# Optimization experiments

Hardware: AMD Instinct MI355X
Metric: run time of the kernel (lower is better)

Reference implementation:

```python
import jax, jax.numpy as jnp
import numpy as np

B, N, K, CIN, COUT, H = 4, 2048, 32, 16, 32, 32
EPS = 1e-5


def setup_inputs() -> dict:
    key = jax.random.key(0)
    ks = jax.random.split(key, 6)
    s = 0.1
    return dict(
        xyz=jax.random.uniform(ks[0], (B, N, 3), dtype=jnp.float32),
        points=jax.random.normal(ks[1], (B, N, CIN), dtype=jnp.float32),
        W1=jax.random.normal(ks[2], (3, H), dtype=jnp.float32) * s,
        b1=jnp.zeros((H,), jnp.float32),
        g1=jnp.ones((H,), jnp.float32),
        be1=jnp.zeros((H,), jnp.float32),
        W2=jax.random.normal(ks[3], (H, H), dtype=jnp.float32) * s,
        b2=jnp.zeros((H,), jnp.float32),
        g2=jnp.ones((H,), jnp.float32),
        be2=jnp.zeros((H,), jnp.float32),
        W3=jax.random.normal(ks[4], (H, CIN * COUT), dtype=jnp.float32) * s,
        b3=jnp.zeros((CIN * COUT,), jnp.float32),
        gbn=jnp.ones((COUT,), jnp.float32),
        bbn=jnp.zeros((COUT,), jnp.float32),
    )


def _bn(h, g, b):
    # BatchNorm1d training-mode math: biased batch stats over axis 0
    return g * (h - h.mean(0)) / jnp.sqrt(h.var(0) + EPS) + b


def reference(xyz, points, W1, b1, g1, be1, W2, b2, g2, be2, W3, b3, gbn, bbn):
    # KNN: squared distances (B,N,N)
    sq = jnp.sum(xyz * xyz, -1)
    dist = -2.0 * jnp.einsum('bmc,bnc->bmn', xyz, xyz) + sq[:, :, None] + sq[:, None, :]
    _, idx = jax.lax.top_k(-dist, K)  # (B,N,K) nearest neighbors

    gather = jax.vmap(lambda p, i: p[i])  # (N,C),(N,K)->(N,K,C), vmapped over B
    grouped_xyz = gather(xyz, idx)                      # (B,N,K,3)
    rel = grouped_xyz - xyz[:, :, None, :]              # (B,N,K,3)
    grouped_pts = gather(points, idx)                   # (B,N,K,CIN)

    # weight net on relative coords
    h = rel.reshape(-1, 3)
    h = _bn(jax.nn.relu(h @ W1 + b1), g1, be1)
    h = _bn(jax.nn.relu(h @ W2 + b2), g2, be2)
    w = (h @ W3 + b3).reshape(B, N, K, CIN, COUT)       # (B,N,K,CIN,COUT)

    # weighted sum over C_in, then max over neighbors
    out = jnp.einsum('bnkc,bnkco->bnko', grouped_pts, w)  # (B,N,K,COUT)
    out = out.max(axis=2)                                 # (B,N,COUT)

    # final BatchNorm1d over (B,N) per channel
    m = out.mean((0, 1))
    v = out.var((0, 1))
    return gbn * (out - m) / jnp.sqrt(v + EPS) + bbn
```

## Files before the change

kernel.cpp:

```cpp
#include <hip/hip_runtime.h>

#define B_ 4
#define N_ 2048
#define K_ 32
#define CIN_ 16
#define COUT_ 32
#define H_ 32
#define R_ (B_*N_*K_)
#define EPS_ 1e-5f
#define INVR_ (1.0f/(float)R_)
#define INVBN_ (1.0f/(float)(B_*N_))
#define LISTCAP 192

typedef __attribute__((ext_vector_type(8)))  _Float16 f16x8;
typedef __attribute__((ext_vector_type(2)))  __fp16   hw16x2;
typedef __attribute__((ext_vector_type(2)))  _Float16 f16x2;
typedef __attribute__((ext_vector_type(16))) float    f32x16;

__device__ __forceinline__ float dot3f(float ax,float ay,float az,float bx,float by,float bz){
    return fmaf(az,bz, fmaf(ay,by, ax*bx));
}
__device__ __forceinline__ unsigned int flip_f32(float d){
    unsigned int u = __float_as_uint(d);
    return u ^ ((unsigned int)(((int)u) >> 31) | 0x80000000u);
}
__device__ __forceinline__ unsigned int pk2(float a, float b){
    union { hw16x2 v; unsigned int u; } c;
    c.v = __builtin_amdgcn_cvt_pkrtz(a, b);
    return c.u;
}
__device__ __forceinline__ unsigned int pkmul(unsigned int a, unsigned int b){
    union { unsigned int u; f16x2 v; } x, y, r;
    x.u = a; y.u = b; r.v = x.v * y.v; return r.u;
}
__device__ __forceinline__ float sh8(const float* __restrict__ p, int k){
    float s = 0.f;
    #pragma unroll
    for (int i = 0; i < 8; ++i) s += p[i*32 + k];
    return s;
}

__device__ __forceinline__ void hsel4(const unsigned int* hq , int lane,
                                      unsigned int Kthr, int* Bsel, unsigned int* below){
    unsigned int g[4];
    #pragma unroll
    for (int t = 0; t < 4; ++t){
        uint4 h = ((const uint4*)hq)[4*lane + t];
        g[t] = h.x + h.y + h.z + h.w;
    }
    unsigned int gs = g[0]+g[1]+g[2]+g[3], cum = gs;
    #pragma unroll
    for (int off = 1; off < 64; off <<= 1){
        unsigned int v = __shfl_up(cum, off);
        if (lane >= off) cum += v;
    }
    unsigned long long bal = __ballot(cum >= Kthr);
    int L = __ffsll(bal) - 1;
    unsigned int run = __shfl(cum, L) - __shfl(gs, L);
    unsigned int h0 = __shfl(g[0], L), h1 = __shfl(g[1], L), h2 = __shfl(g[2], L);
    if      (run + h0 >= Kthr)           { *Bsel = 4*L;     *below = run; }
    else if (run + h0 + h1 >= Kthr)      { *Bsel = 4*L + 1; *below = run + h0; }
    else if (run + h0 + h1 + h2 >= Kthr) { *Bsel = 4*L + 2; *below = run + h0 + h1; }
    else                                 { *Bsel = 4*L + 3; *below = run + h0 + h1 + h2; }
}

__global__ __launch_bounds__(256) void k_prep0(const float* __restrict__ xyz, float4* __restrict__ xs4g,
                                               float* __restrict__ st){
    int i = blockIdx.x*256 + threadIdx.x;
    float x = xyz[3*i], y = xyz[3*i+1], z = xyz[3*i+2];
    xs4g[i] = make_float4(x, y, z, dot3f(x,y,z,x,y,z));
    if (blockIdx.x == 0){
        for (int j = threadIdx.x; j < 640; j += 256) st[j] = 0.f;
    }
}

__global__ __launch_bounds__(256) void k_knn(const float4* __restrict__ xs4g,
                                             const float* __restrict__ W1, const float* __restrict__ b1,
                                             int* __restrict__ idx_out,
                                             float* __restrict__ s1sh, float* __restrict__ q1sh){
    __shared__ unsigned int hist[2][256][4];
    __shared__ unsigned long long lst[2][LISTCAP];
    __shared__ int kidx[2][K_];
    __shared__ unsigned int cnt[2];
    __shared__ float sacc[H_], qacc[H_];

    const int tid  = threadIdx.x;
    const int w    = tid >> 6;
    const int lane = tid & 63;
    const int qi   = w >> 1;
    const int lq   = tid & 127;
    const int b    = blockIdx.x / (N_/2);
    const int q    = (blockIdx.x % (N_/2)) * 2 + qi;
    const int bN   = b * N_;

    for (int i = tid; i < 2048; i += 256) ((unsigned int*)hist)[i] = 0u;
    if (tid < 2) cnt[tid] = 0u;
    if (tid < H_){ sacc[tid] = 0.f; qacc[tid] = 0.f; }
    __syncthreads();

    const float4 qp = xs4g[bN + q];
    const float qx = qp.x, qy = qp.y, qz = qp.z, sqq = qp.w;

    unsigned int fv[16];
    #pragma unroll
    for (int j = 0; j < 16; ++j){
        int c = j*128 + lq;
        float4 pt = xs4g[bN + c];
        float d = fmaf(-2.0f, dot3f(qx,qy,qz, pt.x,pt.y,pt.z), sqq) + pt.w;
        unsigned int f = flip_f32(d);
        fv[j] = f;
        atomicAdd(&hist[qi][f >> 24][lane & 3], 1u);
    }
    __syncthreads();

    int B0; unsigned int lt0;
    hsel4(&hist[qi][0][0], lane, (unsigned)K_, &B0, &lt0);
    unsigned int Kp = (unsigned)K_ - lt0;
    __syncthreads();

    for (int i = tid; i < 2048; i += 256) ((unsigned int*)hist)[i] = 0u;
    __syncthreads();

    #pragma unroll
    for (int j = 0; j < 16; ++j){
        if ((int)(fv[j] >> 24) == B0)
            atomicAdd(&hist[qi][(fv[j] >> 16) & 0xFF][lane & 3], 1u);
    }
    __syncthreads();

    int B1s; unsigned int lt1;
    hsel4(&hist[qi][0][0], lane, Kp, &B1s, &lt1);

    const unsigned long long mlt = (lane == 63) ? ~0ull >> 1 : (1ull << lane) - 1ull;
    #pragma unroll
    for (int j = 0; j < 16; ++j){
        unsigned int f = fv[j];
        int top = (int)(f >> 24);
        bool surv = (top < B0) || (top == B0 && (int)((f >> 16) & 0xFF) <= B1s);
        unsigned long long sb = __ballot(surv);
        if (sb){
            unsigned int t = (unsigned int)__popcll(sb);
            unsigned int base;
            if (lane == 0) base = atomicAdd(&cnt[qi], t);
            base = __shfl(base, 0, 64);
            unsigned int pos = base + (unsigned int)__popcll(sb & mlt);
            if (surv && pos < (unsigned)LISTCAP)
                lst[qi][pos] = ((unsigned long long)f << 32) | (unsigned int)(j*128 + lq);
        }
    }
    __syncthreads();

    int m = (int)cnt[qi]; if (m > LISTCAP) m = LISTCAP;

    int* outp = idx_out + ((size_t)bN + q) * K_;
    for (int i = lq; i < m; i += 128){
        unsigned long long my = lst[qi][i];
        int rank = 0;
        for (int jj = 0; jj < m; ++jj)
            rank += (lst[qi][jj] < my) ? 1 : 0;
        if (rank < K_){
            int id = (int)(unsigned int)(my & 0xFFFFFFFFull);
            outp[rank] = id;
            kidx[qi][rank] = id;
        }
    }
    __syncthreads();

    {
        const int ch = lq & 31, rg = lq >> 5;
        float w1a = W1[ch], w1b = W1[H_+ch], w1c = W1[2*H_+ch], b1c = b1[ch];
        float s = 0.f, qq = 0.f;
        #pragma unroll
        for (int r = 0; r < 8; ++r){
            int id = kidx[qi][rg*8 + r];
            float4 pn = xs4g[bN + id];
            float rx = pn.x - qx, ry = pn.y - qy, rz = pn.z - qz;
            float h = fmaxf(fmaf(rx, w1a, fmaf(ry, w1b, fmaf(rz, w1c, b1c))), 0.0f);
            s += h; qq = fmaf(h, h, qq);
        }
        s  += __shfl_xor(s, 32, 64);
        qq += __shfl_xor(qq, 32, 64);
        if (lane < 32){ atomicAdd(&sacc[lane], s); atomicAdd(&qacc[lane], qq); }
    }
    __syncthreads();
    if (tid < H_){
        int sh = (blockIdx.x & 7) * 32 + tid;
        atomicAdd(&s1sh[sh], sacc[tid]);
        atomicAdd(&q1sh[sh], qacc[tid]);
    }
}

__device__ __forceinline__ void compute_h1(const float* __restrict__ xyz, const int* __restrict__ idx, int r,
                                           const float* __restrict__ W1, const float* __restrict__ b1, float* h1){
    int b = r >> 16;
    int n = (r >> 5) & (N_-1);
    int id = idx[r];
    const float* pc = xyz + ((size_t)b*N_ + n)*3;
    const float* pn = xyz + ((size_t)b*N_ + id)*3;
    float rx = pn[0]-pc[0], ry = pn[1]-pc[1], rz = pn[2]-pc[2];
    #pragma unroll
    for (int j = 0; j < H_; ++j){
        float a = fmaf(rx, W1[j], fmaf(ry, W1[H_+j], fmaf(rz, W1[2*H_+j], b1[j])));
        h1[j] = fmaxf(a, 0.0f);
    }
}

__global__ __launch_bounds__(256) void k_prep2(const float* __restrict__ points,
                                               const float* __restrict__ s1s, const float* __restrict__ q1s,
                                               const float* __restrict__ g1, const float* __restrict__ be1,
                                               const float* __restrict__ W2, const float* __restrict__ b2,
                                               unsigned int* __restrict__ pf16, unsigned int* __restrict__ W2f,
                                               float* __restrict__ b2p){
    int flat = blockIdx.x*256 + threadIdx.x;
    if (flat < 65536){
        pf16[flat] = pk2(points[2*flat], points[2*flat+1]);
    } else if (flat < 66048){
        int d = flat - 65536;
        int jj = d & 3, lane = (d >> 2) & 63, step = d >> 8;
        int col = lane & 31;
        int k0 = step*16 + (lane >> 5)*8 + 2*jj;
        float m0 = sh8(s1s,k0)*INVR_,   v0 = sh8(q1s,k0)*INVR_   - m0*m0;
        float m1 = sh8(s1s,k0+1)*INVR_, v1 = sh8(q1s,k0+1)*INVR_ - m1*m1;
        float a0  = g1[k0]   / sqrtf(v0 + EPS_);
        float a1v = g1[k0+1] / sqrtf(v1 + EPS_);
        W2f[d] = pk2(a0*W2[k0*H_ + col], a1v*W2[(k0+1)*H_ + col]);
    } else if (flat < 66080){
        int col = flat - 66048;
        float acc = b2[col];
        #pragma unroll 4
        for (int h = 0; h < H_; ++h){
            float mm = sh8(s1s,h)*INVR_, vv = sh8(q1s,h)*INVR_ - mm*mm;
            float aa = g1[h] / sqrtf(vv + EPS_);
            float bb = fmaf(-aa, mm, be1[h]);
            acc = fmaf(bb, W2[h*H_ + col], acc);
        }
        b2p[col] = acc;
    }
}

__global__ __launch_bounds__(256,3) void k_h2(const float* __restrict__ xyz, const int* __restrict__ idx,
                                              const float* __restrict__ W1, const float* __restrict__ b1,
                                              const uint4* __restrict__ W2f, const float* __restrict__ b2p,
                                              unsigned short* __restrict__ h2g,
                                              float* gsum, float* gsq){
    __shared__ float redS[H_], redQ[H_];
    const int tid = threadIdx.x, lane = tid & 63, w = tid >> 6;
    const int half = lane >> 5, m = lane & 31;
    if (tid < H_){ redS[tid] = 0.f; redQ[tid] = 0.f; }
    __syncthreads();

    int r = blockIdx.x*256 + tid;
    float h1[H_];
    compute_h1(xyz, idx, r, W1, b1, h1);
    unsigned int h1p[16];
    #pragma unroll
    for (int i = 0; i < 16; ++i) h1p[i] = pk2(h1[2*i], h1[2*i+1]);

    union { uint4 u4; f16x8 v; } Bf0, Bf1;
    Bf0.u4 = W2f[lane];
    Bf1.u4 = W2f[64 + lane];
    float b2c = b2p[m];

    const int rB = blockIdx.x*256 + w*64;
    float s = 0.f, q = 0.f;
    #pragma unroll
    for (int t = 0; t < 2; ++t){
        const int src = t*32 + m;
        union { unsigned int u[4]; f16x8 v; } a0, a1f;
        #pragma unroll
        for (int jj = 0; jj < 4; ++jj){
            unsigned int lo = __shfl(h1p[jj],     src, 64);
            unsigned int hi = __shfl(h1p[4 + jj], src, 64);
            a0.u[jj] = half ? hi : lo;
        }
        #pragma unroll
        for (int jj = 0; jj < 4; ++jj){
            unsigned int lo = __shfl(h1p[8 + jj],  src, 64);
            unsigned int hi = __shfl(h1p[12 + jj], src, 64);
            a1f.u[jj] = half ? hi : lo;
        }
        f32x16 acc;
        #pragma unroll
        for (int i = 0; i < 16; ++i) acc[i] = b2c;
        acc = __builtin_amdgcn_mfma_f32_32x32x16_f16(a0.v,  Bf0.v, acc, 0, 0, 0);
        acc = __builtin_amdgcn_mfma_f32_32x32x16_f16(a1f.v, Bf1.v, acc, 0, 0, 0);
        #pragma unroll
        for (int i = 0; i < 16; ++i){
            float v = fmaxf(acc[i], 0.0f);
            int row = rB + t*32 + (i & 3) + 8*(i >> 2) + 4*half;
            union { _Float16 h; unsigned short u; } cv; cv.h = (_Float16)v;
            h2g[(size_t)row*H_ + m] = cv.u;
            s += v; q = fmaf(v, v, q);
        }
    }
    s += __shfl_xor(s, 32, 64);
    q += __shfl_xor(q, 32, 64);
    if (lane < 32){ atomicAdd(&redS[m], s); atomicAdd(&redQ[m], q); }
    __syncthreads();
    if (tid < H_){ atomicAdd(&gsum[tid], redS[tid]); atomicAdd(&gsq[tid], redQ[tid]); }
}

__global__ __launch_bounds__(256) void k_prep3(const float* __restrict__ W3, const float* __restrict__ b3,
                                               const float* __restrict__ s2, const float* __restrict__ q2,
                                               const float* __restrict__ g2, const float* __restrict__ be2,
                                               unsigned int* __restrict__ W3f){
    int d = blockIdx.x*256 + threadIdx.x;
    int jj = d & 3, lane = (d >> 2) & 63, step = d >> 8;
    int col = lane & 31;
    int off = (lane >> 5)*8 + 2*jj;
    float v0, v1;
    if (step < 32){
        int h = step, c0 = off;
        float mm = s2[h]*INVR_, vv = q2[h]*INVR_ - mm*mm;
        float aa = g2[h] / sqrtf(vv + EPS_);
        v0 = aa * W3[h*512 + c0*COUT_ + col];
        v1 = aa * W3[h*512 + (c0+1)*COUT_ + col];
    } else {
        int c0 = off;
        v0 = b3[c0*COUT_ + col]; v1 = b3[(c0+1)*COUT_ + col];
        #pragma unroll 4
        for (int h = 0; h < H_; ++h){
            float mm = s2[h]*INVR_, vv = q2[h]*INVR_ - mm*mm;
            float aa = g2[h] / sqrtf(vv + EPS_);
            float bb = fmaf(-aa, mm, be2[h]);
            v0 = fmaf(bb, W3[h*512 + c0*COUT_ + col], v0);
            v1 = fmaf(bb, W3[h*512 + (c0+1)*COUT_ + col], v1);
        }
    }
    W3f[d] = pk2(v0, v1);
}

__global__ __launch_bounds__(256,3) void k_out(const int* __restrict__ idx,
                                               const unsigned int* __restrict__ pf16,
                                               const unsigned int* __restrict__ h2u,
                                               const uint4* __restrict__ W3f,
                                               float* __restrict__ out_pre, float* gsum, float* gsq){
    __shared__ float redS[COUT_], redQ[COUT_];
    const int tid = threadIdx.x, lane = tid & 63, w = tid >> 6;
    const int half = lane >> 5, m = lane & 31;
    if (tid < COUT_){ redS[tid] = 0.f; redQ[tid] = 0.f; }
    __syncthreads();

    const int rB = blockIdx.x*256 + w*64;
    const uint4* Wf = W3f + lane;

    #pragma unroll
    for (int t = 0; t < 2; ++t){
        int row = rB + t*32 + m;
        int b = row >> 16;
        int id = idx[row];
        const uint4* gpp = (const uint4*)(pf16 + ((size_t)b*N_ + id)*8);
        uint4 ga = gpp[0], gb = gpp[1];
        unsigned int gsel[4];
        gsel[0] = half ? gb.x : ga.x;
        gsel[1] = half ? gb.y : ga.y;
        gsel[2] = half ? gb.z : ga.z;
        gsel[3] = half ? gb.w : ga.w;
        const uint4* hp = (const uint4*)(h2u + (size_t)row*16);
        uint4 hA = hp[0], hB = hp[1], hC = hp[2], hD = hp[3];
        unsigned int h2p[16] = {hA.x,hA.y,hA.z,hA.w, hB.x,hB.y,hB.z,hB.w,
                                hC.x,hC.y,hC.z,hC.w, hD.x,hD.y,hD.z,hD.w};
        f32x16 acc;
        #pragma unroll
        for (int i = 0; i < 16; ++i) acc[i] = 0.f;

        #pragma unroll
        for (int kb = 0; kb < 32; ++kb){
            unsigned int hr = h2p[kb >> 1];
            unsigned int hd = __builtin_amdgcn_perm(hr, hr, (kb & 1) ? 0x03020302u : 0x01000100u);
            union { unsigned int u[4]; f16x8 v; } af;
            #pragma unroll
            for (int jj = 0; jj < 4; ++jj) af.u[jj] = pkmul(hd, gsel[jj]);
            union { uint4 u4; f16x8 v; } bf; bf.u4 = Wf[kb*64];
            acc = __builtin_amdgcn_mfma_f32_32x32x16_f16(af.v, bf.v, acc, 0, 0, 0);
        }
        {
            union { unsigned int u[4]; f16x8 v; } af;
            #pragma unroll
            for (int jj = 0; jj < 4; ++jj) af.u[jj] = gsel[jj];
            union { uint4 u4; f16x8 v; } bf; bf.u4 = Wf[32*64];
            acc = __builtin_amdgcn_mfma_f32_32x32x16_f16(af.v, bf.v, acc, 0, 0, 0);
        }

        float v = acc[0];
        #pragma unroll
        for (int i = 1; i < 16; ++i) v = fmaxf(v, acc[i]);
        v = fmaxf(v, __shfl_xor(v, 32, 64));
        if (lane < 32){
            int g = blockIdx.x*8 + w*2 + t;
            out_pre[(size_t)g*COUT_ + m] = v;
            atomicAdd(&redS[m], v);
            atomicAdd(&redQ[m], v*v);
        }
    }
    __syncthreads();
    if (tid < COUT_){ atomicAdd(&gsum[tid], redS[tid]); atomicAdd(&gsq[tid], redQ[tid]); }
}

__global__ __launch_bounds__(256) void k_bn(const float* __restrict__ out_pre,
                                            const float* __restrict__ s3, const float* __restrict__ q3,
                                            const float* __restrict__ gbn, const float* __restrict__ bbn,
                                            float* __restrict__ out){
    int i = blockIdx.x*256 + threadIdx.x;
    int o = i & (COUT_-1);
    float mm = s3[o] * INVBN_;
    float vv = q3[o] * INVBN_ - mm*mm;
    float aa = gbn[o] / sqrtf(vv + EPS_);
    out[i] = fmaf(aa, out_pre[i], fmaf(-aa, mm, bbn[o]));
}

extern "C" void kernel_launch(void* const* d_in, const int* in_sizes, int n_in,
                              void* d_out, int out_size, void* d_ws, size_t ws_size,
                              hipStream_t stream){
    const float* xyz    = (const float*)d_in[0];
    const float* points = (const float*)d_in[1];
    const float* W1  = (const float*)d_in[2];
    const float* b1  = (const float*)d_in[3];
    const float* g1  = (const float*)d_in[4];
    const float* be1 = (const float*)d_in[5];
    const float* W2  = (const float*)d_in[6];
    const float* b2  = (const float*)d_in[7];
    const float* g2  = (const float*)d_in[8];
    const float* be2 = (const float*)d_in[9];
    const float* W3  = (const float*)d_in[10];
    const float* b3  = (const float*)d_in[11];
    const float* gbn = (const float*)d_in[12];
    const float* bbn = (const float*)d_in[13];
    float* out = (float*)d_out;

    char* base = (char*)d_ws;
    int*            idx     = (int*)(base + 0);
    float*          out_pre = (float*)(base + 1048576);
    unsigned short* h2g     = (unsigned short*)(base + 2097152);
    unsigned int*   pf16    = (unsigned int*)(base + 18874368);
    unsigned int*   W3f     = (unsigned int*)(base + 19136512);
    unsigned int*   W2f     = (unsigned int*)(base + 19170304);
    float*          b2p     = (float*)(base + 19172352);
    float*          st      = (float*)(base + 19172480);
    float4*         xs4g    = (float4*)(base + 19175040);
    float *s1s=st, *q1s=st+256, *s2=st+512, *q2=st+544, *s3=st+576, *q3=st+608;

    hipLaunchKernelGGL(k_prep0,  dim3(32),          dim3(256), 0, stream, xyz, xs4g, st);
    hipLaunchKernelGGL(k_knn,    dim3(B_*N_/2),     dim3(256), 0, stream, xs4g, W1, b1, idx, s1s, q1s);
    hipLaunchKernelGGL(k_prep2,  dim3(260),         dim3(256), 0, stream, points, s1s, q1s, g1, be1, W2, b2,
                       pf16, W2f, b2p);
    hipLaunchKernelGGL(k_h2,     dim3(R_/256),      dim3(256), 0, stream, xyz, idx, W1, b1,
                       (const uint4*)W2f, b2p, h2g, s2, q2);
    hipLaunchKernelGGL(k_prep3,  dim3(33),          dim3(256), 0, stream, W3, b3, s2, q2, g2, be2, W3f);
    hipLaunchKernelGGL(k_out,    dim3(R_/256),      dim3(256), 0, stream, idx, pf16, (const unsigned int*)h2g,
                       (const uint4*)W3f, out_pre, s3, q3);
    hipLaunchKernelGGL(k_bn,     dim3(B_*N_*COUT_/256), dim3(256), 0, stream, out_pre, s3, q3, gbn, bbn, out);
}
```

Before: 186.9 us.

## Recompute h2 in output kernel and run one KNN query per wavefront

The h2 kernel no longer writes the fp16 hidden activations (R×32 halves) to global memory. Only their BN statistics are kept, and the output kernel recomputes h1 and h2 with MFMA from the neighbor coordinates, so the roughly 16 MB round trip disappears. The KNN kernel now gives each wavefront its own query, with per-wave histograms, and drops block barriers and the shared-memory atomic counter. Stats sharding goes from 8 to 16 shards to cut atomic contention. The cost is duplicated layer-1/layer-2 compute and higher register pressure in k_out.

Result: faster. 180.4 us (-3.4%).

```diff
diff --git a/kernel.cpp b/kernel.cpp
--- a/kernel.cpp
+++ b/kernel.cpp
@@ -11,6 +11,7 @@
 #define INVR_ (1.0f/(float)R_)
 #define INVBN_ (1.0f/(float)(B_*N_))
 #define LISTCAP 192
+#define NSH 16
 
 typedef __attribute__((ext_vector_type(8)))  _Float16 f16x8;
 typedef __attribute__((ext_vector_type(2)))  __fp16   hw16x2;
@@ -33,10 +34,10 @@
     union { unsigned int u; f16x2 v; } x, y, r;
     x.u = a; y.u = b; r.v = x.v * y.v; return r.u;
 }
-__device__ __forceinline__ float sh8(const float* __restrict__ p, int k){
+__device__ __forceinline__ float shsum(const float* __restrict__ p, int k){
     float s = 0.f;
     #pragma unroll
-    for (int i = 0; i < 8; ++i) s += p[i*32 + k];
+    for (int i = 0; i < NSH; ++i) s += p[i*32 + k];
     return s;
 }
 
@@ -70,134 +71,114 @@
     float x = xyz[3*i], y = xyz[3*i+1], z = xyz[3*i+2];
     xs4g[i] = make_float4(x, y, z, dot3f(x,y,z,x,y,z));
     if (blockIdx.x == 0){
-        for (int j = threadIdx.x; j < 640; j += 256) st[j] = 0.f;
-    }
-}
-
-__global__ __launch_bounds__(256) void k_knn(const float4* __restrict__ xs4g,
-                                             const float* __restrict__ W1, const float* __restrict__ b1,
-                                             int* __restrict__ idx_out,
-                                             float* __restrict__ s1sh, float* __restrict__ q1sh){
-    __shared__ unsigned int hist[2][256][4];
-    __shared__ unsigned long long lst[2][LISTCAP];
-    __shared__ int kidx[2][K_];
-    __shared__ unsigned int cnt[2];
-    __shared__ float sacc[H_], qacc[H_];
+        for (int j = threadIdx.x; j < 1152; j += 256) st[j] = 0.f;
+    }
+}
+
+__global__ __launch_bounds__(256,4) void k_knn(const float4* __restrict__ xs4g,
+                                               const float* __restrict__ W1, const float* __restrict__ b1,
+                                               int* __restrict__ idx_out,
+                                               float* __restrict__ s1sh, float* __restrict__ q1sh){
+    __shared__ uint4 hist4[4][256];
+    __shared__ unsigned long long lst[4][LISTCAP];
+    __shared__ int kidx[4][K_];
 
     const int tid  = threadIdx.x;
     const int w    = tid >> 6;
     const int lane = tid & 63;
-    const int qi   = w >> 1;
-    const int lq   = tid & 127;
-    const int b    = blockIdx.x / (N_/2);
-    const int q    = (blockIdx.x % (N_/2)) * 2 + qi;
+    const int half = lane >> 5;
+    const int b    = blockIdx.x >> 9;
+    const int q    = ((blockIdx.x & 511) << 2) + w;
     const int bN   = b * N_;
-
-    for (int i = tid; i < 2048; i += 256) ((unsigned int*)hist)[i] = 0u;
-    if (tid < 2) cnt[tid] = 0u;
-    if (tid < H_){ sacc[tid] = 0.f; qacc[tid] = 0.f; }
-    __syncthreads();
+    unsigned int* hw = (unsigned int*)hist4[w];
+
+    const uint4 z4 = make_uint4(0,0,0,0);
+    hist4[w][lane] = z4; hist4[w][64+lane] = z4; hist4[w][128+lane] = z4; hist4[w][192+lane] = z4;
 
     const float4 qp = xs4g[bN + q];
     const float qx = qp.x, qy = qp.y, qz = qp.z, sqq = qp.w;
 
-    unsigned int fv[16];
-    #pragma unroll
-    for (int j = 0; j < 16; ++j){
-        int c = j*128 + lq;
+    unsigned int fv[32];
+    #pragma unroll
+    for (int j = 0; j < 32; ++j){
+        int c = j*64 + lane;
         float4 pt = xs4g[bN + c];
         float d = fmaf(-2.0f, dot3f(qx,qy,qz, pt.x,pt.y,pt.z), sqq) + pt.w;
         unsigned int f = flip_f32(d);
         fv[j] = f;
-        atomicAdd(&hist[qi][f >> 24][lane & 3], 1u);
-    }
-    __syncthreads();
-
+        atomicAdd(&hw[(f >> 24)*4 + (lane & 3)], 1u);
+    }
     int B0; unsigned int lt0;
-    hsel4(&hist[qi][0][0], lane, (unsigned)K_, &B0, &lt0);
+    hsel4(hw, lane, (unsigned)K_, &B0, &lt0);
     unsigned int Kp = (unsigned)K_ - lt0;
-    __syncthreads();
-
-    for (int i = tid; i < 2048; i += 256) ((unsigned int*)hist)[i] = 0u;
-    __syncthreads();
-
-    #pragma unroll
-    for (int j = 0; j < 16; ++j){
+
+    hist4[w][lane] = z4; hist4[w][64+lane] = z4; hist4[w][128+lane] = z4; hist4[w][192+lane] = z4;
+    #pragma unroll
+    for (int j = 0; j < 32; ++j){
         if ((int)(fv[j] >> 24) == B0)
-            atomicAdd(&hist[qi][(fv[j] >> 16) & 0xFF][lane & 3], 1u);
-    }
-    __syncthreads();
-
+            atomicAdd(&hw[((fv[j] >> 16) & 0xFF)*4 + (lane & 3)], 1u);
+    }
     int B1s; unsigned int lt1;
-    hsel4(&hist[qi][0][0], lane, Kp, &B1s, &lt1);
+    hsel4(hw, lane, Kp, &B1s, &lt1);
 
     const unsigned long long mlt = (lane == 63) ? ~0ull >> 1 : (1ull << lane) - 1ull;
-    #pragma unroll
-    for (int j = 0; j < 16; ++j){
+    unsigned int cnt = 0;
+    #pragma unroll
+    for (int j = 0; j < 32; ++j){
         unsigned int f = fv[j];
         int top = (int)(f >> 24);
         bool surv = (top < B0) || (top == B0 && (int)((f >> 16) & 0xFF) <= B1s);
         unsigned long long sb = __ballot(surv);
-        if (sb){
-            unsigned int t = (unsigned int)__popcll(sb);
-            unsigned int base;
-            if (lane == 0) base = atomicAdd(&cnt[qi], t);
-            base = __shfl(base, 0, 64);
-            unsigned int pos = base + (unsigned int)__popcll(sb & mlt);
-            if (surv && pos < (unsigned)LISTCAP)
-                lst[qi][pos] = ((unsigned long long)f << 32) | (unsigned int)(j*128 + lq);
-        }
-    }
-    __syncthreads();
-
-    int m = (int)cnt[qi]; if (m > LISTCAP) m = LISTCAP;
+        unsigned int pos = cnt + (unsigned int)__popcll(sb & mlt);
+        if (surv && pos < (unsigned)LISTCAP)
+            lst[w][pos] = ((unsigned long long)f << 32) | (unsigned int)(j*64 + lane);
+        cnt += (unsigned int)__popcll(sb);
+    }
+    int m = (int)cnt; if (m > LISTCAP) m = LISTCAP;
 
     int* outp = idx_out + ((size_t)bN + q) * K_;
-    for (int i = lq; i < m; i += 128){
-        unsigned long long my = lst[qi][i];
+    for (int i = lane; i < m; i += 64){
+        unsigned long long my = lst[w][i];
         int rank = 0;
         for (int jj = 0; jj < m; ++jj)
-            rank += (lst[qi][jj] < my) ? 1 : 0;
+            rank += (lst[w][jj] < my) ? 1 : 0;
         if (rank < K_){
             int id = (int)(unsigned int)(my & 0xFFFFFFFFull);
             outp[rank] = id;
-            kidx[qi][rank] = id;
-        }
-    }
-    __syncthreads();
+            kidx[w][rank] = id;
+        }
+    }
 
     {
-        const int ch = lq & 31, rg = lq >> 5;
+        const int ch = lane & 31;
         float w1a = W1[ch], w1b = W1[H_+ch], w1c = W1[2*H_+ch], b1c = b1[ch];
         float s = 0.f, qq = 0.f;
         #pragma unroll
-        for (int r = 0; r < 8; ++r){
-            int id = kidx[qi][rg*8 + r];
-            float4 pn = xs4g[bN + id];
+        for (int r = 0; r < 16; ++r){
+            int idr = kidx[w][half*16 + r];
+            float4 pn = xs4g[bN + idr];
             float rx = pn.x - qx, ry = pn.y - qy, rz = pn.z - qz;
             float h = fmaxf(fmaf(rx, w1a, fmaf(ry, w1b, fmaf(rz, w1c, b1c))), 0.0f);
             s += h; qq = fmaf(h, h, qq);
         }
         s  += __shfl_xor(s, 32, 64);
         qq += __shfl_xor(qq, 32, 64);
-        if (lane < 32){ atomicAdd(&sacc[lane], s); atomicAdd(&qacc[lane], qq); }
-    }
-    __syncthreads();
-    if (tid < H_){
-        int sh = (blockIdx.x & 7) * 32 + tid;
-        atomicAdd(&s1sh[sh], sacc[tid]);
-        atomicAdd(&q1sh[sh], qacc[tid]);
-    }
-}
-
-__device__ __forceinline__ void compute_h1(const float* __restrict__ xyz, const int* __restrict__ idx, int r,
-                                           const float* __restrict__ W1, const float* __restrict__ b1, float* h1){
+        if (lane < 32){
+            int sh = (blockIdx.x & (NSH-1)) * 32 + ch;
+            atomicAdd(&s1sh[sh], s);
+            atomicAdd(&q1sh[sh], qq);
+        }
+    }
+}
+
+__device__ __forceinline__ void compute_h1v(const float4* __restrict__ xs4g, const int* __restrict__ idx, int r,
+                                            const float* __restrict__ W1, const float* __restrict__ b1, float* h1){
     int b = r >> 16;
     int n = (r >> 5) & (N_-1);
     int id = idx[r];
-    const float* pc = xyz + ((size_t)b*N_ + n)*3;
-    const float* pn = xyz + ((size_t)b*N_ + id)*3;
-    float rx = pn[0]-pc[0], ry = pn[1]-pc[1], rz = pn[2]-pc[2];
+    float4 pc = xs4g[b*N_ + n];
+    float4 pn = xs4g[b*N_ + id];
+    float rx = pn.x - pc.x, ry = pn.y - pc.y, rz = pn.z - pc.z;
     #pragma unroll
     for (int j = 0; j < H_; ++j){
         float a = fmaf(rx, W1[j], fmaf(ry, W1[H_+j], fmaf(rz, W1[2*H_+j], b1[j])));
@@ -216,11 +197,11 @@
         pf16[flat] = pk2(points[2*flat], points[2*flat+1]);
     } else if (flat < 66048){
         int d = flat - 65536;
-        int jj = d & 3, lane = (d >> 2) & 63, step = d >> 8;
+        int jj = d & 3, lane = (d >> 2) & 63, s = d >> 8;
         int col = lane & 31;
-        int k0 = step*16 + (lane >> 5)*8 + 2*jj;
-        float m0 = sh8(s1s,k0)*INVR_,   v0 = sh8(q1s,k0)*INVR_   - m0*m0;
-        float m1 = sh8(s1s,k0+1)*INVR_, v1 = sh8(q1s,k0+1)*INVR_ - m1*m1;
+        int k0 = s*16 + (lane >> 5)*8 + 2*jj;
+        float m0 = shsum(s1s,k0)*INVR_,   v0 = shsum(q1s,k0)*INVR_   - m0*m0;
+        float m1 = shsum(s1s,k0+1)*INVR_, v1 = shsum(q1s,k0+1)*INVR_ - m1*m1;
         float a0  = g1[k0]   / sqrtf(v0 + EPS_);
         float a1v = g1[k0+1] / sqrtf(v1 + EPS_);
         W2f[d] = pk2(a0*W2[k0*H_ + col], a1v*W2[(k0+1)*H_ + col]);
@@ -229,7 +210,7 @@
         float acc = b2[col];
         #pragma unroll 4
         for (int h = 0; h < H_; ++h){
-            float mm = sh8(s1s,h)*INVR_, vv = sh8(q1s,h)*INVR_ - mm*mm;
+            float mm = shsum(s1s,h)*INVR_, vv = shsum(q1s,h)*INVR_ - mm*mm;
             float aa = g1[h] / sqrtf(vv + EPS_);
             float bb = fmaf(-aa, mm, be1[h]);
             acc = fmaf(bb, W2[h*H_ + col], acc);
@@ -238,11 +219,10 @@
     }
 }
 
-__global__ __launch_bounds__(256,3) void k_h2(const float* __restrict__ xyz, const int* __restrict__ idx,
-                                              const float* __restrict__ W1, const float* __restrict__ b1,
-                                              const uint4* __restrict__ W2f, const float* __restrict__ b2p,
-                                              unsigned short* __restrict__ h2g,
-                                              float* gsum, float* gsq){
+__global__ __launch_bounds__(256,3) void k_h2stats(const float4* __restrict__ xs4g, const int* __restrict__ idx,
+                                                   const float* __restrict__ W1, const float* __restrict__ b1,
+                                                   const uint4* __restrict__ W2f, const float* __restrict__ b2p,
+                                                   float* gsum, float* gsq){
     __shared__ float redS[H_], redQ[H_];
     const int tid = threadIdx.x, lane = tid & 63, w = tid >> 6;
     const int half = lane >> 5, m = lane & 31;
@@ -251,7 +231,7 @@
 
     int r = blockIdx.x*256 + tid;
     float h1[H_];
-    compute_h1(xyz, idx, r, W1, b1, h1);
+    compute_h1v(xs4g, idx, r, W1, b1, h1);
     unsigned int h1p[16];
     #pragma unroll
     for (int i = 0; i < 16; ++i) h1p[i] = pk2(h1[2*i], h1[2*i+1]);
@@ -261,7 +241,6 @@
     Bf1.u4 = W2f[64 + lane];
     float b2c = b2p[m];
 
-    const int rB = blockIdx.x*256 + w*64;
     float s = 0.f, q = 0.f;
     #pragma unroll
     for (int t = 0; t < 2; ++t){
@@ -287,9 +266,6 @@
         #pragma unroll
         for (int i = 0; i < 16; ++i){
             float v = fmaxf(acc[i], 0.0f);
-            int row = rB + t*32 + (i & 3) + 8*(i >> 2) + 4*half;
-            union { _Float16 h; unsigned short u; } cv; cv.h = (_Float16)v;
-            h2g[(size_t)row*H_ + m] = cv.u;
             s += v; q = fmaf(v, v, q);
         }
     }
@@ -330,9 +306,10 @@
     W3f[d] = pk2(v0, v1);
 }
 
-__global__ __launch_bounds__(256,3) void k_out(const int* __restrict__ idx,
+__global__ __launch_bounds__(256,3) void k_out(const float4* __restrict__ xs4g, const int* __restrict__ idx,
+                                               const float* __restrict__ W1, const float* __restrict__ b1,
+                                               const uint4* __restrict__ W2f, const float* __restrict__ b2p,
                                                const unsigned int* __restrict__ pf16,
-                                               const unsigned int* __restrict__ h2u,
                                                const uint4* __restrict__ W3f,
                                                float* __restrict__ out_pre, float* gsum, float* gsq){
     __shared__ float redS[COUT_], redQ[COUT_];
@@ -342,28 +319,71 @@
     __syncthreads();
 
     const int rB = blockIdx.x*256 + w*64;
+    int r = blockIdx.x*256 + tid;
+
+    float h1[H_];
+    compute_h1v(xs4g, idx, r, W1, b1, h1);
+    unsigned int h1p[16];
+    #pragma unroll
+    for (int i = 0; i < 16; ++i) h1p[i] = pk2(h1[2*i], h1[2*i+1]);
+
+    union { uint4 u4; f16x8 v; } A0, A1;
+    A0.u4 = W2f[lane];
+    A1.u4 = W2f[64 + lane];
+    float b2v[16];
+    #pragma unroll
+    for (int i = 0; i < 16; ++i) b2v[i] = b2p[(i&3) + 8*(i>>2) + 4*half];
+
     const uint4* Wf = W3f + lane;
 
     #pragma unroll
     for (int t = 0; t < 2; ++t){
+        const int src = t*32 + m;
+        union { unsigned int u[4]; f16x8 v; } B0f, B1f;
+        #pragma unroll
+        for (int jj = 0; jj < 4; ++jj){
+            unsigned int lo = __shfl(h1p[jj],     src, 64);
+            unsigned int hi = __shfl(h1p[4 + jj], src, 64);
+            B0f.u[jj] = half ? hi : lo;
+        }
+        #pragma unroll
+        for (int jj = 0; jj < 4; ++jj){
+            unsigned int lo = __shfl(h1p[8 + jj],  src, 64);
+            unsigned int hi = __shfl(h1p[12 + jj], src, 64);
+            B1f.u[jj] = half ? hi : lo;
+        }
+        f32x16 c2;
+        #pragma unroll
+        for (int i = 0; i < 16; ++i) c2[i] = b2v[i];
+        c2 = __builtin_amdgcn_mfma_f32_32x32x16_f16(A0.v, B0f.v, c2, 0, 0, 0);
+        c2 = __builtin_amdgcn_mfma_f32_32x32x16_f16(A1.v, B1f.v, c2, 0, 0, 0);
+
+        unsigned int h2p[16];
+        #pragma unroll
+        for (int p = 0; p < 8; ++p){
+            float v0 = fmaxf(c2[2*p],   0.0f);
+            float v1 = fmaxf(c2[2*p+1], 0.0f);
+            unsigned int ow = pk2(v0, v1);
+            unsigned int ot = __shfl_xor(ow, 32, 64);
+            int a = p >> 1, bb = p & 1;
+            h2p[4*a + 2*half     + bb] = ow;
+            h2p[4*a + 2*(1-half) + bb] = ot;
+        }
+
         int row = rB + t*32 + m;
-        int b = row >> 16;
-        int id = idx[row];
-        const uint4* gpp = (const uint4*)(pf16 + ((size_t)b*N_ + id)*8);
+        int bb_ = row >> 16;
+        int idr = idx[row];
+        const uint4* gpp = (const uint4*)(pf16 + ((size_t)bb_*N_ + idr)*8);
         uint4 ga = gpp[0], gb = gpp[1];
         unsigned int gsel[4];
         gsel[0] = half ? gb.x : ga.x;
         gsel[1] = half ? gb.y : ga.y;
         gsel[2] = half ? gb.z : ga.z;
         gsel[3] = half ? gb.w : ga.w;
-        const uint4* hp = (const uint4*)(h2u + (size_t)row*16);
-        uint4 hA = hp[0], hB = hp[1], hC = hp[2], hD = hp[3];
-        unsigned int h2p[16] = {hA.x,hA.y,hA.z,hA.w, hB.x,hB.y,hB.z,hB.w,
-                                hC.x,hC.y,hC.z,hC.w, hD.x,hD.y,hD.z,hD.w};
+
         f32x16 acc;
         #pragma unroll
         for (int i = 0; i < 16; ++i) acc[i] = 0.f;
-
         #pragma unroll
         for (int kb = 0; kb < 32; ++kb){
             unsigned int hr = h2p[kb >> 1];
@@ -431,23 +451,22 @@
     char* base = (char*)d_ws;
     int*            idx     = (int*)(base + 0);
     float*          out_pre = (float*)(base + 1048576);
-    unsigned short* h2g     = (unsigned short*)(base + 2097152);
-    unsigned int*   pf16    = (unsigned int*)(base + 18874368);
-    unsigned int*   W3f     = (unsigned int*)(base + 19136512);
-    unsigned int*   W2f     = (unsigned int*)(base + 19170304);
-    float*          b2p     = (float*)(base + 19172352);
-    float*          st      = (float*)(base + 19172480);
-    float4*         xs4g    = (float4*)(base + 19175040);
-    float *s1s=st, *q1s=st+256, *s2=st+512, *q2=st+544, *s3=st+576, *q3=st+608;
-
-    hipLaunchKernelGGL(k_prep0,  dim3(32),          dim3(256), 0, stream, xyz, xs4g, st);
-    hipLaunchKernelGGL(k_knn,    dim3(B_*N_/2),     dim3(256), 0, stream, xs4g, W1, b1, idx, s1s, q1s);
-    hipLaunchKernelGGL(k_prep2,  dim3(260),         dim3(256), 0, stream, points, s1s, q1s, g1, be1, W2, b2,
+    unsigned int*   pf16    = (unsigned int*)(base + 2097152);
+    unsigned int*   W3f     = (unsigned int*)(base + 2359296);
+    unsigned int*   W2f     = (unsigned int*)(base + 2393088);
+    float*          b2p     = (float*)(base + 2395136);
+    float*          st      = (float*)(base + 2395264);
+    float4*         xs4g    = (float4*)(base + 2399872);
+    float *s1s=st, *q1s=st+512, *s2=st+1024, *q2=st+1056, *s3=st+1088, *q3=st+1120;
+
+    hipLaunchKernelGGL(k_prep0,   dim3(32),      dim3(256), 0, stream, xyz, xs4g, st);
+    hipLaunchKernelGGL(k_knn,     dim3(B_*N_/4), dim3(256), 0, stream, xs4g, W1, b1, idx, s1s, q1s);
+    hipLaunchKernelGGL(k_prep2,   dim3(260),     dim3(256), 0, stream, points, s1s, q1s, g1, be1, W2, b2,
                        pf16, W2f, b2p);
-    hipLaunchKernelGGL(k_h2,     dim3(R_/256),      dim3(256), 0, stream, xyz, idx, W1, b1,
-                       (const uint4*)W2f, b2p, h2g, s2, q2);
-    hipLaunchKernelGGL(k_prep3,  dim3(33),          dim3(256), 0, stream, W3, b3, s2, q2, g2, be2, W3f);
-    hipLaunchKernelGGL(k_out,    dim3(R_/256),      dim3(256), 0, stream, idx, pf16, (const unsigned int*)h2g,
-                       (const uint4*)W3f, out_pre, s3, q3);
-    hipLaunchKernelGGL(k_bn,     dim3(B_*N_*COUT_/256), dim3(256), 0, stream, out_pre, s3, q3, gbn, bbn, out);
-}
+    hipLaunchKernelGGL(k_h2stats, dim3(R_/256),  dim3(256), 0, stream, xs4g, idx, W1, b1,
+                       (const uint4*)W2f, b2p, s2, q2);
+    hipLaunchKernelGGL(k_prep3,   dim3(33),      dim3(256), 0, stream, W3, b3, s2, q2, g2, be2, W3f);
+    hipLaunchKernelGGL(k_out,     dim3(R_/256),  dim3(256), 0, stream, xs4g, idx, W1, b1,
+                       (const uint4*)W2f, b2p, pf16, (const uint4*)W3f, out_pre, s3, q3);
+    hipLaunchKernelGGL(k_bn,      dim3(B_*N_*COUT_/256), dim3(256), 0, stream, out_pre, s3, q3, gbn, bbn, out);
+}
```
